# Kernel optimization log

Hardware: AMD Instinct MI355X
Metric: run time of the kernel (lower is better)

## Reference

```python
import jax, jax.numpy as jnp
import numpy as np

B, C, H, W = 4, 128, 64, 64


def setup_inputs() -> dict:
    key = jax.random.key(0)
    ks = jax.random.split(key, 8)
    return {
        "x": jax.random.normal(ks[0], (B, C, H, W), dtype=jnp.float32),
        "Wq": jax.random.normal(ks[1], (C // 4, C), dtype=jnp.float32) * 0.05,
        "bq": jax.random.normal(ks[2], (C // 4,), dtype=jnp.float32) * 0.05,
        "Wk": jax.random.normal(ks[3], (C // 4, C), dtype=jnp.float32) * 0.05,
        "bk": jax.random.normal(ks[4], (C // 4,), dtype=jnp.float32) * 0.05,
        "Wv": jax.random.normal(ks[5], (C, C), dtype=jnp.float32) * 0.05,
        "bv": jax.random.normal(ks[6], (C,), dtype=jnp.float32) * 0.05,
        "gamma": jnp.full((1,), 0.1, dtype=jnp.float32),
        "pos": jax.random.normal(ks[7], (1, C, 32, 32), dtype=jnp.float32) * 0.02,
    }


def reference(x, Wq, bq, Wk, bk, Wv, bv, gamma, pos):
    b, c, h, w = x.shape
    n = h * w
    # bilinear upsample of position encoding (half-pixel centers = torch align_corners=False)
    pe = jax.image.resize(pos, (1, c, h, w), method="bilinear")
    scale_factor = min(1.0, 16.0 / max(h, w))  # static shapes -> python float
    xp = x + scale_factor * 0.1 * pe
    # 1x1 conv projections as einsums; q/k: [b, c/4, n], v: [b, c, n]
    q = (jnp.einsum("bchw,oc->bohw", xp, Wq) + bq[None, :, None, None]).reshape(b, -1, n)
    k = (jnp.einsum("bchw,oc->bohw", xp, Wk) + bk[None, :, None, None]).reshape(b, -1, n)
    v = (jnp.einsum("bchw,oc->bohw", xp, Wv) + bv[None, :, None, None]).reshape(b, c, n)
    # scores[b, i, j] = <q_i, k_j> / (sqrt(C) + eps); softmax over j
    scores = jnp.einsum("bdn,bdm->bnm", q, k) / (c ** 0.5 + 1e-08)
    attn = jax.nn.softmax(scores, axis=-1)
    # out = V @ attn^T  -> [b, c, n]
    out = jnp.einsum("bcn,bmn->bcm", v, attn).reshape(b, c, h, w)
    return gamma[0] * out + xp
```

## Files before the change

### kernel.cpp

```cpp
#include <hip/hip_runtime.h>
#include <hip/hip_bf16.h>
#include <cstdint>
#include <cstddef>

typedef __attribute__((ext_vector_type(8))) short bf16x8;
typedef __attribute__((ext_vector_type(4))) float f32x4;
typedef __attribute__((ext_vector_type(16))) float f32x16;
typedef __attribute__((ext_vector_type(2))) unsigned int u32x2;
typedef unsigned int u32;
typedef unsigned short u16;
typedef unsigned char u8;

__device__ __forceinline__ u16 f2bf(float f) {
  union { float f; u32 u; } v; v.f = f;
  u32 r = v.u + 0x7FFFu + ((v.u >> 16) & 1u);
  return (u16)(r >> 16);
}
__device__ __forceinline__ u32 pk2(float a, float b) {
  return (u32)f2bf(a) | ((u32)f2bf(b) << 16);
}
__device__ __forceinline__ float bfhi(u32 u) {
  union { u32 u; float f; } v; v.u = u & 0xFFFF0000u; return v.f;
}
__device__ __forceinline__ float bflo(u32 u) {
  union { u32 u; float f; } v; v.u = u << 16; return v.f;
}
__device__ __forceinline__ float fexp2(float x) {
  return __builtin_amdgcn_exp2f(x);
}

struct ProjArgs {
  const u16* tbrow;
};

__device__ __forceinline__ void proj_tile(int mts, int li, int g,
    const u16* tb, int tb_stride_u16, int n0, int b,
    const float* Wq, const float* bq, const float* Wk, const float* bk,
    const float* Wv, const float* bv,
    u16* qw, u16* kw, u8* v2) {
  const float qscale = 0.088388347648318447f * 1.4426950408889634f;
  int row = mts * 16 + li;
  const float* wsrc = row < 32 ? Wq + (size_t)row * 128
                    : row < 64 ? Wk + (size_t)(row - 32) * 128
                               : Wv + (size_t)(row - 64) * 128;
  int ob = mts * 16 + g * 4;
  const float* bsrc = ob < 32 ? bq + ob : ob < 64 ? bk + (ob - 32) : bv + (ob - 64);
  f32x4 acc[4];
#pragma unroll
  for (int nt = 0; nt < 4; ++nt) acc[nt] = (f32x4){0.f, 0.f, 0.f, 0.f};
#pragma unroll
  for (int kc = 0; kc < 4; ++kc) {
    float4 wa = *(const float4*)(wsrc + kc * 32 + g * 8);
    float4 wb = *(const float4*)(wsrc + kc * 32 + g * 8 + 4);
    union { u32 u[4]; bf16x8 v; } af;
    af.u[0] = pk2(wa.x, wa.y); af.u[1] = pk2(wa.z, wa.w);
    af.u[2] = pk2(wb.x, wb.y); af.u[3] = pk2(wb.z, wb.w);
    bf16x8 bfr[4];
#pragma unroll
    for (int nt = 0; nt < 4; ++nt)
      bfr[nt] = *(const bf16x8*)(tb + (size_t)(nt * 16 + li) * tb_stride_u16 + kc * 32 + g * 8);
#pragma unroll
    for (int nt = 0; nt < 4; ++nt)
      acc[nt] = __builtin_amdgcn_mfma_f32_16x16x32_bf16(af.v, bfr[nt], acc[nt], 0, 0, 0);
  }
  float bias[4];
#pragma unroll
  for (int r = 0; r < 4; ++r) bias[r] = bsrc[r];
#pragma unroll
  for (int nt = 0; nt < 4; ++nt) {
    int n = n0 + nt * 16 + li;
    float v0 = acc[nt][0] + bias[0];
    float v1 = acc[nt][1] + bias[1];
    float v2v = acc[nt][2] + bias[2];
    float v3 = acc[nt][3] + bias[3];
    if (mts < 2) {
      v0 *= qscale; v1 *= qscale; v2v *= qscale; v3 *= qscale;
      uint2 pk; pk.x = pk2(v0, v1); pk.y = pk2(v2v, v3);
      *(uint2*)(qw + (((size_t)b * 4096) + n) * 32 + ob) = pk;
    } else if (mts < 4) {
      uint2 pk; pk.x = pk2(v0, v1); pk.y = pk2(v2v, v3);
      *(uint2*)(kw + (((size_t)b * 4096) + n) * 32 + (ob - 32)) = pk;
    } else {
      int cv = ob - 64;
      u32 w01 = (u32)__builtin_amdgcn_cvt_pk_fp8_f32(v0, v1, 0, false);
      u32 w23 = (u32)__builtin_amdgcn_cvt_pk_fp8_f32(v2v, v3, 0, false);
      size_t vb = (((size_t)b * 128 + (n >> 5)) * 128 + cv) * 32 + (n & 31);
      v2[vb]      = (u8)(w01 & 0xFF);
      v2[vb + 32] = (u8)((w01 >> 8) & 0xFF);
      v2[vb + 64] = (u8)(w23 & 0xFF);
      v2[vb + 96] = (u8)((w23 >> 8) & 0xFF);
    }
  }
}

__global__ __launch_bounds__(512) void k_pp(const float* __restrict__ x,
    const float* __restrict__ pos,
    const float* __restrict__ Wq, const float* __restrict__ bq,
    const float* __restrict__ Wk, const float* __restrict__ bk,
    const float* __restrict__ Wv, const float* __restrict__ bv,
    float* __restrict__ xp,
    u16* __restrict__ qw, u16* __restrict__ kw, u8* __restrict__ v2) {
  __shared__ float tf[128][66];
  __shared__ u16 tb[64][136];
  int t = threadIdx.x;
  int n0 = blockIdx.x * 64;
  int b = blockIdx.y;
  int h = blockIdx.x;
  int hj = h >> 1;
  int ya, yb; float wa, wb;
  if ((h & 1) == 0) { ya = hj - 1 < 0 ? 0 : hj - 1; yb = hj; wa = 0.25f; wb = 0.75f; }
  else             { ya = hj; yb = hj + 1 > 31 ? 31 : hj + 1; wa = 0.75f; wb = 0.25f; }
  {
    int cl = t >> 2, q4 = t & 3;
    int w0 = q4 * 16;
    const float* pr0 = pos + (size_t)cl * 1024 + ya * 32;
    const float* pr1 = pos + (size_t)cl * 1024 + yb * 32;
    int i0 = q4 * 8;
    float rr[10];
#pragma unroll
    for (int j = 0; j < 10; ++j) {
      int idx = i0 - 1 + j;
      idx = idx < 0 ? 0 : (idx > 31 ? 31 : idx);
      rr[j] = wa * pr0[idx] + wb * pr1[idx];
    }
    size_t gbase = ((size_t)(b * 128 + cl)) * 4096 + h * 64 + w0;
#pragma unroll
    for (int u = 0; u < 4; ++u) {
      float4 xv = *(const float4*)(x + gbase + u * 4);
      float vals[4] = {xv.x, xv.y, xv.z, xv.w};
#pragma unroll
      for (int j = 0; j < 4; ++j) {
        int e = u * 4 + j;
        int li = (e >> 1) + 1;
        float pe = (e & 1) == 0 ? 0.25f * rr[li - 1] + 0.75f * rr[li]
                                : 0.75f * rr[li] + 0.25f * rr[li + 1];
        float xe = vals[j] + 0.025f * pe;
        vals[j] = xe;
        tf[cl][w0 + e] = xe;
      }
      float4 st = {vals[0], vals[1], vals[2], vals[3]};
      *(float4*)(xp + gbase + u * 4) = st;
    }
  }
  __syncthreads();
  {
    int nl = t & 63, qr = t >> 6;
    u32* tbw = (u32*)&tb[0][0];
#pragma unroll
    for (int p = 0; p < 8; ++p)
      tbw[nl * 68 + qr * 8 + p] =
          pk2(tf[qr * 16 + 2 * p][nl], tf[qr * 16 + 2 * p + 1][nl]);
  }
  __syncthreads();
  int wv = t >> 6, lane = t & 63, li = lane & 15, g = lane >> 4;
  proj_tile(wv, li, g, &tb[0][0], 136, n0, b, Wq, bq, Wk, bk, Wv, bv, qw, kw, v2);
  if (wv < 4)
    proj_tile(8 + wv, li, g, &tb[0][0], 136, n0, b, Wq, bq, Wk, bk, Wv, bv, qw, kw, v2);
}

__global__ __launch_bounds__(512, 2) void k_attn(const u16* __restrict__ qw,
    const u16* __restrict__ kw, const u8* __restrict__ v2,
    const float* __restrict__ xp, const float* __restrict__ gamma,
    float* __restrict__ out) {
  __shared__ u32 buf[4][32][66];
  __shared__ float lm[8][32];
  __shared__ float ll[8][32];
  int t = threadIdx.x;
  int wv = t >> 6, lane = t & 63;
  int q = lane & 31, hi = lane >> 5;
  int b = blockIdx.y;
  int q0 = blockIdx.x * 64;
  const u16* qbase = qw + (((size_t)b * 4096) + q0) * 32 + hi * 8;
  bf16x8 qA0 = *(const bf16x8*)(qbase + (size_t)q * 32);
  bf16x8 qA1 = *(const bf16x8*)(qbase + (size_t)q * 32 + 16);
  bf16x8 qB0 = *(const bf16x8*)(qbase + (size_t)(32 + q) * 32);
  bf16x8 qB1 = *(const bf16x8*)(qbase + (size_t)(32 + q) * 32 + 16);
  f32x16 accA[4] = {}, accB[4] = {};
  const f32x16 zz = {};
  float mA = -1e30f, lA = 0.f, mB = -1e30f, lB = 0.f;
  const u16* kbb = kw + ((size_t)b * 4096) * 32;
  const u8* vbb = v2 + (size_t)b * 524288;
  int kv_beg = wv * 512;
  const u16* kr0 = kbb + (size_t)(kv_beg + q) * 32 + hi * 8;
  bf16x8 kc0 = *(const bf16x8*)kr0;
  bf16x8 kc1 = *(const bf16x8*)(kr0 + 16);

  for (int it = 0; it < 16; ++it) {
    int kv0 = kv_beg + it * 32;
    const u8* vch = vbb + (size_t)(kv0 >> 5) * 4096 + q * 32 + hi * 8;
    uint2 vr[8];
#pragma unroll
    for (int ct = 0; ct < 4; ++ct) {
      vr[2 * ct]     = *(const uint2*)(vch + ct * 1024);
      vr[2 * ct + 1] = *(const uint2*)(vch + ct * 1024 + 16);
    }
    f32x16 sA = __builtin_amdgcn_mfma_f32_32x32x16_bf16(kc0, qA0, zz, 0, 0, 0);
    sA = __builtin_amdgcn_mfma_f32_32x32x16_bf16(kc1, qA1, sA, 0, 0, 0);
    f32x16 sB = __builtin_amdgcn_mfma_f32_32x32x16_bf16(kc0, qB0, zz, 0, 0, 0);
    sB = __builtin_amdgcn_mfma_f32_32x32x16_bf16(kc1, qB1, sB, 0, 0, 0);
    if (it < 15) {
      const u16* krn = kbb + (size_t)(kv0 + 32 + q) * 32 + hi * 8;
      kc0 = *(const bf16x8*)krn;
      kc1 = *(const bf16x8*)(krn + 16);
    }
    float xa0 = fmaxf(fmaxf(sA[0], sA[1]), fmaxf(sA[2], sA[3]));
    float xa1 = fmaxf(fmaxf(sA[4], sA[5]), fmaxf(sA[6], sA[7]));
    float xa2 = fmaxf(fmaxf(sA[8], sA[9]), fmaxf(sA[10], sA[11]));
    float xa3 = fmaxf(fmaxf(sA[12], sA[13]), fmaxf(sA[14], sA[15]));
    float mxA = fmaxf(fmaxf(xa0, xa1), fmaxf(xa2, xa3));
    float xb0 = fmaxf(fmaxf(sB[0], sB[1]), fmaxf(sB[2], sB[3]));
    float xb1 = fmaxf(fmaxf(sB[4], sB[5]), fmaxf(sB[6], sB[7]));
    float xb2 = fmaxf(fmaxf(sB[8], sB[9]), fmaxf(sB[10], sB[11]));
    float xb3 = fmaxf(fmaxf(sB[12], sB[13]), fmaxf(sB[14], sB[15]));
    float mxB = fmaxf(fmaxf(xb0, xb1), fmaxf(xb2, xb3));
    {
      union { float f; u32 u; } ca, cb;
      ca.f = mxA; cb.f = mxB;
      u32x2 swa = __builtin_amdgcn_permlane32_swap(ca.u, ca.u, false, false);
      u32x2 swb = __builtin_amdgcn_permlane32_swap(cb.u, cb.u, false, false);
      union { u32 u; float f; } r0, r1;
      r0.u = swa[0]; r1.u = swa[1]; mxA = fmaxf(r0.f, r1.f);
      r0.u = swb[0]; r1.u = swb[1]; mxB = fmaxf(r0.f, r1.f);
    }
    bool ok = (mxA <= mA + 8.f) && (mxB <= mB + 8.f);
    if (!__all(ok)) {
      float mnA = fmaxf(mA, mxA), mnB = fmaxf(mB, mxB);
      float aA = fexp2(mA - mnA), aB = fexp2(mB - mnB);
      lA *= aA; lB *= aB;
#pragma unroll
      for (int ct = 0; ct < 4; ++ct)
#pragma unroll
        for (int r = 0; r < 16; ++r) {
          accA[ct][r] *= aA;
          accB[ct][r] *= aB;
        }
      mA = mnA; mB = mnB;
    }
    {
      float p[16];
#pragma unroll
      for (int r = 0; r < 16; ++r) p[r] = fexp2(sA[r] - mA);
      float s0 = (p[0] + p[1]) + (p[2] + p[3]);
      float s1 = (p[4] + p[5]) + (p[6] + p[7]);
      float s2 = (p[8] + p[9]) + (p[10] + p[11]);
      float s3 = (p[12] + p[13]) + (p[14] + p[15]);
      float sum = (s0 + s1) + (s2 + s3);
      union { float f; u32 u; } cv; cv.f = sum;
      u32x2 sw = __builtin_amdgcn_permlane32_swap(cv.u, cv.u, false, false);
      union { u32 u; float f; } r0, r1; r0.u = sw[0]; r1.u = sw[1];
      lA += r0.f + r1.f;
      u32 dw0 = (u32)__builtin_amdgcn_cvt_pk_fp8_f32(p[0], p[1], 0, false);
      dw0 = (u32)__builtin_amdgcn_cvt_pk_fp8_f32(p[2], p[3], (int)dw0, true);
      u32 dw1 = (u32)__builtin_amdgcn_cvt_pk_fp8_f32(p[4], p[5], 0, false);
      dw1 = (u32)__builtin_amdgcn_cvt_pk_fp8_f32(p[6], p[7], (int)dw1, true);
      u32 dw2 = (u32)__builtin_amdgcn_cvt_pk_fp8_f32(p[8], p[9], 0, false);
      dw2 = (u32)__builtin_amdgcn_cvt_pk_fp8_f32(p[10], p[11], (int)dw2, true);
      u32 dw3 = (u32)__builtin_amdgcn_cvt_pk_fp8_f32(p[12], p[13], 0, false);
      dw3 = (u32)__builtin_amdgcn_cvt_pk_fp8_f32(p[14], p[15], (int)dw3, true);
      u32x2 sw0 = __builtin_amdgcn_permlane32_swap(dw0, dw1, false, false);
      u32x2 sw1 = __builtin_amdgcn_permlane32_swap(dw2, dw3, false, false);
      union { uint2 u; long long l_; } pf0, pf1;
      pf0.u.x = sw0[0]; pf0.u.y = sw0[1];
      pf1.u.x = sw1[0]; pf1.u.y = sw1[1];
#pragma unroll
      for (int ct = 0; ct < 4; ++ct) {
        union { uint2 u; long long l_; } v0u, v1u;
        v0u.u = vr[2 * ct]; v1u.u = vr[2 * ct + 1];
        accA[ct] = __builtin_amdgcn_mfma_f32_32x32x16_fp8_fp8(v0u.l_, pf0.l_, accA[ct], 0, 0, 0);
        accA[ct] = __builtin_amdgcn_mfma_f32_32x32x16_fp8_fp8(v1u.l_, pf1.l_, accA[ct], 0, 0, 0);
      }
    }
    {
      float p[16];
#pragma unroll
      for (int r = 0; r < 16; ++r) p[r] = fexp2(sB[r] - mB);
      float s0 = (p[0] + p[1]) + (p[2] + p[3]);
      float s1 = (p[4] + p[5]) + (p[6] + p[7]);
      float s2 = (p[8] + p[9]) + (p[10] + p[11]);
      float s3 = (p[12] + p[13]) + (p[14] + p[15]);
      float sum = (s0 + s1) + (s2 + s3);
      union { float f; u32 u; } cv; cv.f = sum;
      u32x2 sw = __builtin_amdgcn_permlane32_swap(cv.u, cv.u, false, false);
      union { u32 u; float f; } r0, r1; r0.u = sw[0]; r1.u = sw[1];
      lB += r0.f + r1.f;
      u32 dw0 = (u32)__builtin_amdgcn_cvt_pk_fp8_f32(p[0], p[1], 0, false);
      dw0 = (u32)__builtin_amdgcn_cvt_pk_fp8_f32(p[2], p[3], (int)dw0, true);
      u32 dw1 = (u32)__builtin_amdgcn_cvt_pk_fp8_f32(p[4], p[5], 0, false);
      dw1 = (u32)__builtin_amdgcn_cvt_pk_fp8_f32(p[6], p[7], (int)dw1, true);
      u32 dw2 = (u32)__builtin_amdgcn_cvt_pk_fp8_f32(p[8], p[9], 0, false);
      dw2 = (u32)__builtin_amdgcn_cvt_pk_fp8_f32(p[10], p[11], (int)dw2, true);
      u32 dw3 = (u32)__builtin_amdgcn_cvt_pk_fp8_f32(p[12], p[13], 0, false);
      dw3 = (u32)__builtin_amdgcn_cvt_pk_fp8_f32(p[14], p[15], (int)dw3, true);
      u32x2 sw0 = __builtin_amdgcn_permlane32_swap(dw0, dw1, false, false);
      u32x2 sw1 = __builtin_amdgcn_permlane32_swap(dw2, dw3, false, false);
      union { uint2 u; long long l_; } pf0, pf1;
      pf0.u.x = sw0[0]; pf0.u.y = sw0[1];
      pf1.u.x = sw1[0]; pf1.u.y = sw1[1];
#pragma unroll
      for (int ct = 0; ct < 4; ++ct) {
        union { uint2 u; long long l_; } v0u, v1u;
        v0u.u = vr[2 * ct]; v1u.u = vr[2 * ct + 1];
        accB[ct] = __builtin_amdgcn_mfma_f32_32x32x16_fp8_fp8(v0u.l_, pf0.l_, accB[ct], 0, 0, 0);
        accB[ct] = __builtin_amdgcn_mfma_f32_32x32x16_fp8_fp8(v1u.l_, pf1.l_, accB[ct], 0, 0, 0);
      }
    }
  }

  float g0 = gamma[0];
#define COMBINE_PASS(ACC, MV, LV, QOFF)                                       \
  __syncthreads();                                                            \
  if (lane < 32) { lm[wv][q] = MV; ll[wv][q] = LV; }                          \
  if (wv >= 4) {                                                              \
    int w = wv - 4;                                                           \
    _Pragma("unroll")                                                         \
    for (int ct = 0; ct < 4; ++ct)                                            \
      _Pragma("unroll")                                                       \
      for (int q4 = 0; q4 < 4; ++q4) {                                        \
        uint2 pkd;                                                            \
        pkd.x = pk2(ACC[ct][q4 * 4 + 0], ACC[ct][q4 * 4 + 1]);                \
        pkd.y = pk2(ACC[ct][q4 * 4 + 2], ACC[ct][q4 * 4 + 3]);                \
        *(uint2*)&buf[w][q][16 * ct + 4 * q4 + 2 * hi] = pkd;                 \
      }                                                                       \
  }                                                                           \
  __syncthreads();                                                            \
  if (wv < 4) {                                                               \
    float m2 = lm[wv + 4][q], l2 = ll[wv + 4][q];                             \
    float mm = fmaxf(MV, m2);                                                 \
    float fa = fexp2(MV - mm), fb = fexp2(m2 - mm);                           \
    _Pragma("unroll")                                                         \
    for (int ct = 0; ct < 4; ++ct)                                            \
      _Pragma("unroll")                                                       \
      for (int q4 = 0; q4 < 4; ++q4) {                                        \
        uint2 pr = *(const uint2*)&buf[wv][q][16 * ct + 4 * q4 + 2 * hi];     \
        ACC[ct][q4 * 4 + 0] = ACC[ct][q4 * 4 + 0] * fa + bflo(pr.x) * fb;     \
        ACC[ct][q4 * 4 + 1] = ACC[ct][q4 * 4 + 1] * fa + bfhi(pr.x) * fb;     \
        ACC[ct][q4 * 4 + 2] = ACC[ct][q4 * 4 + 2] * fa + bflo(pr.y) * fb;     \
        ACC[ct][q4 * 4 + 3] = ACC[ct][q4 * 4 + 3] * fa + bfhi(pr.y) * fb;     \
      }                                                                       \
    LV = LV * fa + l2 * fb;                                                   \
    MV = mm;                                                                  \
  }                                                                           \
  __syncthreads();                                                            \
  if (wv < 4 && lane < 32) { lm[wv][q] = MV; ll[wv][q] = LV; }                \
  __syncthreads();                                                            \
  if (wv < 4) {                                                               \
    float ms = fmaxf(fmaxf(lm[0][q], lm[1][q]), fmaxf(lm[2][q], lm[3][q]));   \
    float f = fexp2(MV - ms);                                                 \
    _Pragma("unroll")                                                         \
    for (int ct = 0; ct < 4; ++ct)                                            \
      _Pragma("unroll")                                                       \
      for (int q4 = 0; q4 < 4; ++q4) {                                        \
        uint2 pkd;                                                            \
        pkd.x = pk2(ACC[ct][q4 * 4 + 0] * f, ACC[ct][q4 * 4 + 1] * f);        \
        pkd.y = pk2(ACC[ct][q4 * 4 + 2] * f, ACC[ct][q4 * 4 + 3] * f);        \
        *(uint2*)&buf[wv][q][16 * ct + 4 * q4 + 2 * hi] = pkd;                \
      }                                                                       \
  }                                                                           \
  __syncthreads();                                                            \
  {                                                                           \
    int qe = t & 31, cg = t >> 5;                                             \
    float m0 = lm[0][qe], m1 = lm[1][qe], m2 = lm[2][qe], m3 = lm[3][qe];     \
    float ms = fmaxf(fmaxf(m0, m1), fmaxf(m2, m3));                           \
    float ls = ll[0][qe] * fexp2(m0 - ms) + ll[1][qe] * fexp2(m1 - ms)        \
             + ll[2][qe] * fexp2(m2 - ms) + ll[3][qe] * fexp2(m3 - ms);       \
    float inv = 1.f / ls;                                                     \
    float sacc[8];                                                            \
    _Pragma("unroll")                                                         \
    for (int j = 0; j < 8; ++j) sacc[j] = 0.f;                                \
    _Pragma("unroll")                                                         \
    for (int w = 0; w < 4; ++w) {                                             \
      uint4 r = *(const uint4*)&buf[w][qe][cg * 4];                           \
      sacc[0] += bflo(r.x); sacc[1] += bfhi(r.x);                             \
      sacc[2] += bflo(r.y); sacc[3] += bfhi(r.y);                             \
      sacc[4] += bflo(r.z); sacc[5] += bfhi(r.z);                             \
      sacc[6] += bflo(r.w); sacc[7] += bfhi(r.w);                             \
    }                                                                         \
    _Pragma("unroll")                                                         \
    for (int j = 0; j < 8; ++j) {                                             \
      size_t adr = (((size_t)b * 128) + cg * 8 + j) * 4096 + q0 + (QOFF) + qe;\
      out[adr] = g0 * sacc[j] * inv + xp[adr];                                \
    }                                                                         \
  }

  COMBINE_PASS(accA, mA, lA, 0)
  COMBINE_PASS(accB, mB, lB, 32)
#undef COMBINE_PASS
}

extern "C" void kernel_launch(void* const* d_in, const int* in_sizes, int n_in,
                              void* d_out, int out_size, void* d_ws, size_t ws_size,
                              hipStream_t stream) {
  const float* x     = (const float*)d_in[0];
  const float* Wq    = (const float*)d_in[1];
  const float* bq    = (const float*)d_in[2];
  const float* Wk    = (const float*)d_in[3];
  const float* bk    = (const float*)d_in[4];
  const float* Wv    = (const float*)d_in[5];
  const float* bv    = (const float*)d_in[6];
  const float* gamma = (const float*)d_in[7];
  const float* pos   = (const float*)d_in[8];
  float* out = (float*)d_out;

  char* ws = (char*)d_ws;
  float* xp  = (float*)ws;
  u16* qw    = (u16*)(ws + 8388608);
  u16* kw    = (u16*)(ws + 9437184);
  u8*  v2    = (u8*)(ws + 10485760);

  k_pp<<<dim3(64, 4), 512, 0, stream>>>(x, pos, Wq, bq, Wk, bk, Wv, bv,
                                        xp, qw, kw, v2);
  k_attn<<<dim3(64, 4), 512, 0, stream>>>(qw, kw, v2, xp, gamma, out);
}
```

Before: 43.91 us.

## Fuse projection and attention kernels via cooperative grid sync, recompute xp

Merges the preprocessing/projection kernel and the attention kernel into one cooperative kernel separated by a grid-wide barrier, with shared memory aliased between the two phases. The fp32 xp intermediate is no longer written; the epilogue recomputes the bilinear position encoding from pos and adds it to x directly. This removes a kernel launch gap and 8 MB of write plus read traffic for xp. In exchange it pays for a grid barrier, extra gathers from pos in the epilogue, and requires all 256 blocks to be co-resident.

```diff
diff --git a/kernel.cpp b/kernel.cpp
--- a/kernel.cpp
+++ b/kernel.cpp
@@ -1,7 +1,10 @@
 #include <hip/hip_runtime.h>
 #include <hip/hip_bf16.h>
+#include <hip/hip_cooperative_groups.h>
 #include <cstdint>
 #include <cstddef>
+
+namespace cg = cooperative_groups;
 
 typedef __attribute__((ext_vector_type(8))) short bf16x8;
 typedef __attribute__((ext_vector_type(4))) float f32x4;
@@ -28,10 +31,6 @@
 __device__ __forceinline__ float fexp2(float x) {
   return __builtin_amdgcn_exp2f(x);
 }
-
-struct ProjArgs {
-  const u16* tbrow;
-};
 
 __device__ __forceinline__ void proj_tile(int mts, int li, int g,
     const u16* tb, int tb_stride_u16, int n0, int b,
@@ -93,23 +92,30 @@
   }
 }
 
-__global__ __launch_bounds__(512) void k_pp(const float* __restrict__ x,
-    const float* __restrict__ pos,
+__global__ __launch_bounds__(512, 2) void k_fused(
+    const float* __restrict__ x, const float* __restrict__ pos,
     const float* __restrict__ Wq, const float* __restrict__ bq,
     const float* __restrict__ Wk, const float* __restrict__ bk,
     const float* __restrict__ Wv, const float* __restrict__ bv,
-    float* __restrict__ xp,
-    u16* __restrict__ qw, u16* __restrict__ kw, u8* __restrict__ v2) {
-  __shared__ float tf[128][66];
-  __shared__ u16 tb[64][136];
+    const float* __restrict__ gamma,
+    u16* __restrict__ qw, u16* __restrict__ kw, u8* __restrict__ v2,
+    float* __restrict__ out) {
+  __shared__ char smem[51200];
+  float (*tf)[66] = (float(*)[66])smem;
+  u16 (*tb)[136] = (u16(*)[136])(smem + 33792);
+  u32 (*buf)[32][66] = (u32(*)[32][66])smem;
+  float (*lm)[32] = (float(*)[32])(smem + 33792);
+  float (*ll)[32] = (float(*)[32])(smem + 33792 + 1024);
+
   int t = threadIdx.x;
-  int n0 = blockIdx.x * 64;
   int b = blockIdx.y;
-  int h = blockIdx.x;
-  int hj = h >> 1;
-  int ya, yb; float wa, wb;
-  if ((h & 1) == 0) { ya = hj - 1 < 0 ? 0 : hj - 1; yb = hj; wa = 0.25f; wb = 0.75f; }
-  else             { ya = hj; yb = hj + 1 > 31 ? 31 : hj + 1; wa = 0.75f; wb = 0.25f; }
+  int hh = blockIdx.x;
+  int n0 = hh * 64;
+
+  int hj = hh >> 1;
+  int ya, yb; float wya, wyb;
+  if ((hh & 1) == 0) { ya = hj - 1 < 0 ? 0 : hj - 1; yb = hj; wya = 0.25f; wyb = 0.75f; }
+  else              { ya = hj; yb = hj + 1 > 31 ? 31 : hj + 1; wya = 0.75f; wyb = 0.25f; }
   {
     int cl = t >> 2, q4 = t & 3;
     int w0 = q4 * 16;
@@ -121,9 +127,9 @@
     for (int j = 0; j < 10; ++j) {
       int idx = i0 - 1 + j;
       idx = idx < 0 ? 0 : (idx > 31 ? 31 : idx);
-      rr[j] = wa * pr0[idx] + wb * pr1[idx];
-    }
-    size_t gbase = ((size_t)(b * 128 + cl)) * 4096 + h * 64 + w0;
+      rr[j] = wya * pr0[idx] + wyb * pr1[idx];
+    }
+    size_t gbase = ((size_t)(b * 128 + cl)) * 4096 + hh * 64 + w0;
 #pragma unroll
     for (int u = 0; u < 4; ++u) {
       float4 xv = *(const float4*)(x + gbase + u * 4);
@@ -134,12 +140,8 @@
         int li = (e >> 1) + 1;
         float pe = (e & 1) == 0 ? 0.25f * rr[li - 1] + 0.75f * rr[li]
                                 : 0.75f * rr[li] + 0.25f * rr[li + 1];
-        float xe = vals[j] + 0.025f * pe;
-        vals[j] = xe;
-        tf[cl][w0 + e] = xe;
+        tf[cl][w0 + e] = vals[j] + 0.025f * pe;
       }
-      float4 st = {vals[0], vals[1], vals[2], vals[3]};
-      *(float4*)(xp + gbase + u * 4) = st;
     }
   }
   __syncthreads();
@@ -152,24 +154,19 @@
           pk2(tf[qr * 16 + 2 * p][nl], tf[qr * 16 + 2 * p + 1][nl]);
   }
   __syncthreads();
-  int wv = t >> 6, lane = t & 63, li = lane & 15, g = lane >> 4;
-  proj_tile(wv, li, g, &tb[0][0], 136, n0, b, Wq, bq, Wk, bk, Wv, bv, qw, kw, v2);
-  if (wv < 4)
-    proj_tile(8 + wv, li, g, &tb[0][0], 136, n0, b, Wq, bq, Wk, bk, Wv, bv, qw, kw, v2);
-}
-
-__global__ __launch_bounds__(512, 2) void k_attn(const u16* __restrict__ qw,
-    const u16* __restrict__ kw, const u8* __restrict__ v2,
-    const float* __restrict__ xp, const float* __restrict__ gamma,
-    float* __restrict__ out) {
-  __shared__ u32 buf[4][32][66];
-  __shared__ float lm[8][32];
-  __shared__ float ll[8][32];
-  int t = threadIdx.x;
+  {
+    int wv = t >> 6, lane = t & 63, li = lane & 15, g = lane >> 4;
+    proj_tile(wv, li, g, &tb[0][0], 136, n0, b, Wq, bq, Wk, bk, Wv, bv, qw, kw, v2);
+    if (wv < 4)
+      proj_tile(8 + wv, li, g, &tb[0][0], 136, n0, b, Wq, bq, Wk, bk, Wv, bv, qw, kw, v2);
+  }
+
+  __threadfence();
+  cg::this_grid().sync();
+
   int wv = t >> 6, lane = t & 63;
   int q = lane & 31, hi = lane >> 5;
-  int b = blockIdx.y;
-  int q0 = blockIdx.x * 64;
+  int q0 = n0;
   const u16* qbase = qw + (((size_t)b * 4096) + q0) * 32 + hi * 8;
   bf16x8 qA0 = *(const bf16x8*)(qbase + (size_t)q * 32);
   bf16x8 qA1 = *(const bf16x8*)(qbase + (size_t)q * 32 + 16);
@@ -358,7 +355,7 @@
   }                                                                           \
   __syncthreads();                                                            \
   {                                                                           \
-    int qe = t & 31, cg = t >> 5;                                             \
+    int qe = t & 31, cgr = t >> 5;                                            \
     float m0 = lm[0][qe], m1 = lm[1][qe], m2 = lm[2][qe], m3 = lm[3][qe];     \
     float ms = fmaxf(fmaxf(m0, m1), fmaxf(m2, m3));                           \
     float ls = ll[0][qe] * fexp2(m0 - ms) + ll[1][qe] * fexp2(m1 - ms)        \
@@ -369,16 +366,29 @@
     for (int j = 0; j < 8; ++j) sacc[j] = 0.f;                                \
     _Pragma("unroll")                                                         \
     for (int w = 0; w < 4; ++w) {                                             \
-      uint4 r = *(const uint4*)&buf[w][qe][cg * 4];                           \
+      uint4 r = *(const uint4*)&buf[w][qe][cgr * 4];                          \
       sacc[0] += bflo(r.x); sacc[1] += bfhi(r.x);                             \
       sacc[2] += bflo(r.y); sacc[3] += bfhi(r.y);                             \
       sacc[4] += bflo(r.z); sacc[5] += bfhi(r.z);                             \
       sacc[6] += bflo(r.w); sacc[7] += bfhi(r.w);                             \
     }                                                                         \
+    int ww = (QOFF) + qe;                                                     \
+    int wj = ww >> 1;                                                         \
+    int xaI, xbI; float wxa, wxb;                                             \
+    if ((ww & 1) == 0) { xaI = wj - 1 < 0 ? 0 : wj - 1; xbI = wj;             \
+                         wxa = 0.25f; wxb = 0.75f; }                          \
+    else               { xaI = wj; xbI = wj + 1 > 31 ? 31 : wj + 1;           \
+                         wxa = 0.75f; wxb = 0.25f; }                          \
+    int o00 = ya * 32 + xaI, o01 = ya * 32 + xbI;                             \
+    int o10 = yb * 32 + xaI, o11 = yb * 32 + xbI;                             \
     _Pragma("unroll")                                                         \
     for (int j = 0; j < 8; ++j) {                                             \
-      size_t adr = (((size_t)b * 128) + cg * 8 + j) * 4096 + q0 + (QOFF) + qe;\
-      out[adr] = g0 * sacc[j] * inv + xp[adr];                                \
+      int c = cgr * 8 + j;                                                    \
+      const float* pj = pos + (size_t)c * 1024;                               \
+      float pe = wya * (wxa * pj[o00] + wxb * pj[o01])                        \
+               + wyb * (wxa * pj[o10] + wxb * pj[o11]);                       \
+      size_t adr = (((size_t)b * 128) + c) * 4096 + q0 + (QOFF) + qe;         \
+      out[adr] = g0 * sacc[j] * inv + x[adr] + 0.025f * pe;                   \
     }                                                                         \
   }
 
@@ -402,12 +412,15 @@
   float* out = (float*)d_out;
 
   char* ws = (char*)d_ws;
-  float* xp  = (float*)ws;
-  u16* qw    = (u16*)(ws + 8388608);
-  u16* kw    = (u16*)(ws + 9437184);
-  u8*  v2    = (u8*)(ws + 10485760);
-
-  k_pp<<<dim3(64, 4), 512, 0, stream>>>(x, pos, Wq, bq, Wk, bk, Wv, bv,
-                                        xp, qw, kw, v2);
-  k_attn<<<dim3(64, 4), 512, 0, stream>>>(qw, kw, v2, xp, gamma, out);
-}
+  u16* qw = (u16*)ws;
+  u16* kw = (u16*)(ws + 1048576);
+  u8*  v2 = (u8*)(ws + 2097152);
+
+  void* kargs[] = {
+    (void*)&x, (void*)&pos, (void*)&Wq, (void*)&bq, (void*)&Wk, (void*)&bk,
+    (void*)&Wv, (void*)&bv, (void*)&gamma, (void*)&qw, (void*)&kw, (void*)&v2,
+    (void*)&out
+  };
+  hipLaunchCooperativeKernel(reinterpret_cast<void*>(k_fused),
+                             dim3(64, 4), dim3(512), kargs, 0, stream);
+}
```

Result: slower. 147.6 us (+236.2%).
